# Kernel tuning notes

Hardware: AMD Instinct MI355X
Metric: run time of the kernel (lower is better)

Reference implementation:

```python
import jax, jax.numpy as jnp
import numpy as np

NUM_CLASSES = 10000
FEAT_DIM = 1024
BATCH = 4096


def setup_inputs() -> dict:
    key = jax.random.key(0)
    k1, k2 = jax.random.split(key)
    feat = jax.random.normal(k1, (BATCH, FEAT_DIM), dtype=jnp.float32)
    centers = jax.random.normal(k2, (NUM_CLASSES, FEAT_DIM), dtype=jnp.float32)
    return {"feat": feat, "centers": centers}


def reference(feat, centers):
    # logits = -0.5 * ||feat_b - center_c||^2, computed via the GEMM rewrite
    # ||a-b||^2 = ||a||^2 + ||b||^2 - 2 a.b  (same math as broadcast-sub-square-sum,
    # but avoids the [B, C, D] intermediate and uses tensor-core matmul).
    feat_sq = jnp.sum(feat * feat, axis=-1, keepdims=True)          # [B, 1]
    cent_sq = jnp.sum(centers * centers, axis=-1)[None, :]          # [1, C]
    cross = jnp.einsum('bd,cd->bc', feat, centers)                  # [B, C]
    dist = feat_sq + cent_sq - 2.0 * cross                          # [B, C]
    logits = -0.5 * dist
    return logits
```

## Files before the change

### kernel.cpp

```cpp
#include <hip/hip_runtime.h>
#include <hip/hip_bf16.h>
#include <stdint.h>

#define M_DIM 4096
#define N_DIM 10000
#define K_DIM 1024
#define GM (M_DIM / 128)
#define GN ((N_DIM + 127) / 128)
#define SB 16

typedef __attribute__((ext_vector_type(8))) short bf16x8;
typedef __attribute__((ext_vector_type(4))) float f32x4;

#define BAR()      asm volatile("s_barrier" ::: "memory")
#define WAITVM4()  asm volatile("s_waitcnt vmcnt(4)" ::: "memory")
#define WAITVM0()  asm volatile("s_waitcnt vmcnt(0)" ::: "memory")
#define WAITLGKM() asm volatile("s_waitcnt lgkmcnt(0)" ::: "memory")

__device__ __forceinline__ void async_ld16(const void* g, void* l) {
    __builtin_amdgcn_global_load_lds(
        (const __attribute__((address_space(1))) unsigned int*)g,
        (__attribute__((address_space(3))) unsigned int*)l,
        16, 0, 0);
}

__device__ __forceinline__ unsigned short f2bf(float f) {
    unsigned u = __float_as_uint(f);
    unsigned r = (u + 0x7FFFu + ((u >> 16) & 1u)) >> 16;
    return (unsigned short)r;
}

__global__ __launch_bounds__(256) void prep_rows(
    const float* __restrict__ feat, const float* __restrict__ cent,
    unsigned short* __restrict__ featbf, unsigned short* __restrict__ centbf,
    float* __restrict__ fsq, float* __restrict__ csq)
{
    const int wlane = threadIdx.x & 63;
    const int wid   = blockIdx.x * 4 + (threadIdx.x >> 6);
    const int nw    = gridDim.x * 4;
    for (int row = wid; row < M_DIM + N_DIM; row += nw) {
        const float* in;
        unsigned short* outb;
        float* sqp;
        if (row < M_DIM) {
            in = feat + (size_t)row * K_DIM;
            outb = featbf + (size_t)row * K_DIM;
            sqp = fsq + row;
        } else {
            const int r2 = row - M_DIM;
            in = cent + (size_t)r2 * K_DIM;
            outb = centbf + (size_t)r2 * K_DIM;
            sqp = csq + r2;
        }
        float s = 0.f;
        #pragma unroll
        for (int c = 0; c < 4; c++) {
            float4 v = ((const float4*)in)[wlane + c * 64];
            ushort4 pk;
            pk.x = f2bf(v.x); pk.y = f2bf(v.y); pk.z = f2bf(v.z); pk.w = f2bf(v.w);
            ((ushort4*)outb)[wlane + c * 64] = pk;
            s += v.x * v.x + v.y * v.y + v.z * v.z + v.w * v.w;
        }
        #pragma unroll
        for (int off = 32; off > 0; off >>= 1) s += __shfl_down(s, off, 64);
        if (wlane == 0) *sqp = s;
    }
}

__global__ __launch_bounds__(256) void gemm_bt(
    const unsigned short* __restrict__ A,
    const unsigned short* __restrict__ B,
    const float* __restrict__ fsq, const float* __restrict__ csq,
    float* __restrict__ out)
{
    __shared__ unsigned short smem[16384];

    const int tid  = threadIdx.x;
    const int lane = tid & 63;
    const int wave = tid >> 6;
    const int wm = wave & 1, wn = wave >> 1;

    const int lin  = blockIdx.x;
    const int band = lin / (SB * GM);
    const int r0   = lin - band * (SB * GM);
    const int bn0  = band * SB;
    int bw = GN - bn0; if (bw > SB) bw = SB;
    const int bm = r0 / bw;
    const int bn = bn0 + (r0 - bm * bw);

    const int arow_base = bm * 128;
    const int brow_base = bn * 128;

    const int srow = tid >> 2;
    const int scol = (tid & 3) * 8;

    const unsigned short* gA0 = A + (size_t)(arow_base + srow) * K_DIM + scol;
    const unsigned short* gA1 = gA0 + (size_t)64 * K_DIM;
    int br0 = brow_base + srow;      if (br0 > N_DIM - 1) br0 = N_DIM - 1;
    int br1 = brow_base + 64 + srow; if (br1 > N_DIM - 1) br1 = N_DIM - 1;
    const unsigned short* gB0 = B + (size_t)br0 * K_DIM + scol;
    const unsigned short* gB1 = B + (size_t)br1 * K_DIM + scol;

    f32x4 acc[4][4];
    #pragma unroll
    for (int i = 0; i < 4; i++)
        #pragma unroll
        for (int j = 0; j < 4; j++) {
            f32x4 z = {0.f, 0.f, 0.f, 0.f};
            acc[i][j] = z;
        }

    const int mlane = lane & 15;
    const int quad  = lane >> 4;
    const int aoff = (wm * 64 + mlane) * 32 + quad * 8;
    const int boff = 4096 + (wn * 64 + mlane) * 32 + quad * 8;

    async_ld16(gA0, smem + tid * 8);
    async_ld16(gA1, smem + 2048 + tid * 8);
    async_ld16(gB0, smem + 4096 + tid * 8);
    async_ld16(gB1, smem + 6144 + tid * 8);
    gA0 += 32; gA1 += 32; gB0 += 32; gB1 += 32;

    #define COMPUTE(bufbase)                                                  \
        do {                                                                  \
            const unsigned short* ap = smem + (bufbase) + aoff;               \
            const unsigned short* bp = smem + (bufbase) + boff;               \
            bf16x8 af[4], bfv[4];                                             \
            _Pragma("unroll")                                                 \
            for (int i = 0; i < 4; i++) {                                     \
                af[i]  = *(const bf16x8*)(ap + i * 16 * 32);                  \
                bfv[i] = *(const bf16x8*)(bp + i * 16 * 32);                  \
            }                                                                 \
            _Pragma("unroll")                                                 \
            for (int i = 0; i < 4; i++)                                       \
                _Pragma("unroll")                                             \
                for (int j = 0; j < 4; j++)                                   \
                    acc[i][j] = __builtin_amdgcn_mfma_f32_16x16x32_bf16(      \
                        af[i], bfv[j], acc[i][j], 0, 0, 0);                   \
        } while (0)

    for (int kt = 0; kt < K_DIM / 32 - 1; ++kt) {
        const int buf  = kt & 1;
        const int nbase = (buf ^ 1) * 8192;
        async_ld16(gA0, smem + nbase + tid * 8);
        async_ld16(gA1, smem + nbase + 2048 + tid * 8);
        async_ld16(gB0, smem + nbase + 4096 + tid * 8);
        async_ld16(gB1, smem + nbase + 6144 + tid * 8);
        gA0 += 32; gA1 += 32; gB0 += 32; gB1 += 32;
        WAITVM4();
        BAR();
        COMPUTE(buf * 8192);
        BAR();
    }
    WAITVM0();
    BAR();
    COMPUTE(8192);
    BAR();

    float* W = (float*)smem + wave * 1088;
    const int rbase0 = arow_base + wm * 64;
    const int cbase  = brow_base + wn * 64 + mlane;
    const int rb_col4 = mlane * 4;
    const int rb_rows = quad;
    const int gcol4 = brow_base + wn * 64 + rb_col4;
    const bool colok = gcol4 < N_DIM;

    #pragma unroll
    for (int i = 0; i < 4; i++) {
        float frow[4];
        #pragma unroll
        for (int r = 0; r < 4; r++)
            frow[r] = -0.5f * fsq[rbase0 + i * 16 + quad * 4 + r];
        #pragma unroll
        for (int j = 0; j < 4; j++) {
            int col = cbase + j * 16;
            float cs = -0.5f * csq[col < N_DIM ? col : (N_DIM - 1)];
            #pragma unroll
            for (int r = 0; r < 4; r++)
                W[(quad * 4 + r) * 68 + j * 16 + mlane] = acc[i][j][r] + frow[r] + cs;
        }
        WAITLGKM();
        #pragma unroll
        for (int s = 0; s < 4; s++) {
            int rl = s * 4 + rb_rows;
            f32x4 v = *(const f32x4*)&W[rl * 68 + rb_col4];
            if (colok) {
                int grow = rbase0 + i * 16 + rl;
                __builtin_nontemporal_store(v, (f32x4*)&out[(size_t)grow * N_DIM + gcol4]);
            }
        }
        WAITLGKM();
    }
    #undef COMPUTE
}

extern "C" void kernel_launch(void* const* d_in, const int* in_sizes, int n_in,
                              void* d_out, int out_size, void* d_ws, size_t ws_size,
                              hipStream_t stream) {
    const float* feat = (const float*)d_in[0];
    const float* cent = (const float*)d_in[1];
    float* out = (float*)d_out;

    char* ws = (char*)d_ws;
    unsigned short* featbf = (unsigned short*)ws;
    unsigned short* centbf = (unsigned short*)(ws + 8388608);
    float* fsq = (float*)(ws + 8388608 + 20480000);
    float* csq = (float*)(ws + 8388608 + 20480000 + 16384);

    prep_rows<<<1024, 256, 0, stream>>>(feat, cent, featbf, centbf, fsq, csq);

    gemm_bt<<<GM * GN, 256, 0, stream>>>(featbf, centbf, fsq, csq, out);
}
```

Before: 302.0 us.

## Enlarge GEMM tile to 256x256 with 8 waves, triple-buffered swizzled LDS

Switches the bf16 GEMM from 128x128 tiles with 4 waves to 256x256 tiles with 8 waves. It also adds a three-stage LDS ring with XOR-swizzled K offsets to avoid bank conflicts, and splits each K step into two half-compute phases that interleave the A and B prefetches. Blocks are remapped in XCD-aware order, and setprio is raised around the MFMA bursts. The aim is more operand reuse per loaded byte and better overlap of loads with compute. In exchange each block uses 96KB of LDS and more registers, which lowers occupancy. The 256-wide N tiling also wastes more work on the ragged 10000 edge.

After: 293.1 us. -2.9%, faster.

```diff
diff --git a/kernel.cpp b/kernel.cpp
--- a/kernel.cpp
+++ b/kernel.cpp
@@ -5,9 +5,9 @@
 #define M_DIM 4096
 #define N_DIM 10000
 #define K_DIM 1024
-#define GM (M_DIM / 128)
-#define GN ((N_DIM + 127) / 128)
-#define SB 16
+#define GM (M_DIM / 256)
+#define GN ((N_DIM + 255) / 256)
+#define NT (K_DIM / 32)
 
 typedef __attribute__((ext_vector_type(8))) short bf16x8;
 typedef __attribute__((ext_vector_type(4))) float f32x4;
@@ -67,106 +67,136 @@
     }
 }
 
-__global__ __launch_bounds__(256) void gemm_bt(
+__global__ __launch_bounds__(512, 2) void gemm_bt(
     const unsigned short* __restrict__ A,
     const unsigned short* __restrict__ B,
     const float* __restrict__ fsq, const float* __restrict__ csq,
     float* __restrict__ out)
 {
-    __shared__ unsigned short smem[16384];
+    __shared__ unsigned short smem[49152];
 
     const int tid  = threadIdx.x;
     const int lane = tid & 63;
     const int wave = tid >> 6;
-    const int wm = wave & 1, wn = wave >> 1;
-
-    const int lin  = blockIdx.x;
-    const int band = lin / (SB * GM);
-    const int r0   = lin - band * (SB * GM);
-    const int bn0  = band * SB;
-    int bw = GN - bn0; if (bw > SB) bw = SB;
-    const int bm = r0 / bw;
-    const int bn = bn0 + (r0 - bm * bw);
-
-    const int arow_base = bm * 128;
-    const int brow_base = bn * 128;
-
-    const int srow = tid >> 2;
-    const int scol = (tid & 3) * 8;
-
-    const unsigned short* gA0 = A + (size_t)(arow_base + srow) * K_DIM + scol;
-    const unsigned short* gA1 = gA0 + (size_t)64 * K_DIM;
-    int br0 = brow_base + srow;      if (br0 > N_DIM - 1) br0 = N_DIM - 1;
-    int br1 = brow_base + 64 + srow; if (br1 > N_DIM - 1) br1 = N_DIM - 1;
-    const unsigned short* gB0 = B + (size_t)br0 * K_DIM + scol;
-    const unsigned short* gB1 = B + (size_t)br1 * K_DIM + scol;
-
-    f32x4 acc[4][4];
+    const int wm = wave & 1;
+    const int wn = wave >> 1;
+    const int mlane = lane & 15;
+    const int quad  = lane >> 4;
+    const int fr  = (mlane >> 1) & 3;
+    const int qx  = (quad ^ fr) << 4;
+
+    const int bid = blockIdx.x;
+    const int xcd = bid & 7;
+    const int idx = bid >> 3;
+    const int r0  = xcd * 80 + idx;
+    const int bm  = r0 & 15;
+    const int bn  = r0 >> 4;
+
+    const int arow_base = bm * 256;
+    const int brow_base = bn * 256;
+
+    const unsigned short* gA[2];
+    const unsigned short* gB[2];
+    int ldsA[2], ldsB[2];
     #pragma unroll
-    for (int i = 0; i < 4; i++)
+    for (int i = 0; i < 2; i++) {
+        const int s   = i * 512 + tid;
+        const int row = s >> 2;
+        const int sc  = s & 3;
+        const int kof = (sc ^ ((row >> 1) & 3)) << 3;
+        gA[i] = A + (size_t)(arow_base + row) * K_DIM + kof;
+        int br = brow_base + row; if (br > N_DIM - 1) br = N_DIM - 1;
+        gB[i] = B + (size_t)br * K_DIM + kof;
+        ldsA[i] = s * 16;
+        ldsB[i] = 16384 + s * 16;
+    }
+
+    #define STAGE_A(t2, nbb)                                                  \
+        do {                                                                  \
+            async_ld16(gA[0] + (size_t)(t2) * 32, (char*)smem + (nbb) + ldsA[0]); \
+            async_ld16(gA[1] + (size_t)(t2) * 32, (char*)smem + (nbb) + ldsA[1]); \
+        } while (0)
+    #define STAGE_B(t2, nbb)                                                  \
+        do {                                                                  \
+            async_ld16(gB[0] + (size_t)(t2) * 32, (char*)smem + (nbb) + ldsB[0]); \
+            async_ld16(gB[1] + (size_t)(t2) * 32, (char*)smem + (nbb) + ldsB[1]); \
+        } while (0)
+
+    f32x4 acc[8][4];
+    #pragma unroll
+    for (int i = 0; i < 8; i++)
         #pragma unroll
         for (int j = 0; j < 4; j++) {
             f32x4 z = {0.f, 0.f, 0.f, 0.f};
             acc[i][j] = z;
         }
 
-    const int mlane = lane & 15;
-    const int quad  = lane >> 4;
-    const int aoff = (wm * 64 + mlane) * 32 + quad * 8;
-    const int boff = 4096 + (wn * 64 + mlane) * 32 + quad * 8;
-
-    async_ld16(gA0, smem + tid * 8);
-    async_ld16(gA1, smem + 2048 + tid * 8);
-    async_ld16(gB0, smem + 4096 + tid * 8);
-    async_ld16(gB1, smem + 6144 + tid * 8);
-    gA0 += 32; gA1 += 32; gB0 += 32; gB1 += 32;
-
-    #define COMPUTE(bufbase)                                                  \
-        do {                                                                  \
-            const unsigned short* ap = smem + (bufbase) + aoff;               \
-            const unsigned short* bp = smem + (bufbase) + boff;               \
-            bf16x8 af[4], bfv[4];                                             \
-            _Pragma("unroll")                                                 \
-            for (int i = 0; i < 4; i++) {                                     \
-                af[i]  = *(const bf16x8*)(ap + i * 16 * 32);                  \
-                bfv[i] = *(const bf16x8*)(bp + i * 16 * 32);                  \
-            }                                                                 \
-            _Pragma("unroll")                                                 \
-            for (int i = 0; i < 4; i++)                                       \
-                _Pragma("unroll")                                             \
-                for (int j = 0; j < 4; j++)                                   \
-                    acc[i][j] = __builtin_amdgcn_mfma_f32_16x16x32_bf16(      \
-                        af[i], bfv[j], acc[i][j], 0, 0, 0);                   \
-        } while (0)
-
-    for (int kt = 0; kt < K_DIM / 32 - 1; ++kt) {
-        const int buf  = kt & 1;
-        const int nbase = (buf ^ 1) * 8192;
-        async_ld16(gA0, smem + nbase + tid * 8);
-        async_ld16(gA1, smem + nbase + 2048 + tid * 8);
-        async_ld16(gB0, smem + nbase + 4096 + tid * 8);
-        async_ld16(gB1, smem + nbase + 6144 + tid * 8);
-        gA0 += 32; gA1 += 32; gB0 += 32; gB1 += 32;
-        WAITVM4();
-        BAR();
-        COMPUTE(buf * 8192);
-        BAR();
-    }
-    WAITVM0();
+    const int aBase = (wm * 128 + mlane) * 64 + qx;
+    const int bBase = 16384 + (wn * 64 + mlane) * 64 + qx;
+
+    STAGE_A(0, 0); STAGE_B(0, 0);
+    STAGE_A(1, 32768); STAGE_B(1, 32768);
+    WAITVM4();
     BAR();
-    COMPUTE(8192);
-    BAR();
+
+    int bb = 0;
+    for (int t = 0; t < NT; ++t) {
+        int nb = bb - 32768; if (nb < 0) nb = 65536;
+        const char* base = (const char*)smem + bb;
+        bf16x8 af[4], bfv[4];
+
+        #pragma unroll
+        for (int i = 0; i < 4; i++) {
+            af[i]  = *(const bf16x8*)(base + aBase + i * 1024);
+            bfv[i] = *(const bf16x8*)(base + bBase + i * 1024);
+        }
+        if (t + 2 < NT) STAGE_A(t + 2, nb);
+        BAR();
+        WAITLGKM();
+        __builtin_amdgcn_s_setprio(1);
+        #pragma unroll
+        for (int i = 0; i < 4; i++)
+            #pragma unroll
+            for (int j = 0; j < 4; j++)
+                acc[i][j] = __builtin_amdgcn_mfma_f32_16x16x32_bf16(
+                    af[i], bfv[j], acc[i][j], 0, 0, 0);
+        __builtin_amdgcn_s_setprio(0);
+        BAR();
+
+        #pragma unroll
+        for (int i = 0; i < 4; i++)
+            af[i] = *(const bf16x8*)(base + aBase + 4096 + i * 1024);
+        if (t + 2 < NT) STAGE_B(t + 2, nb);
+        BAR();
+        WAITLGKM();
+        __builtin_amdgcn_s_setprio(1);
+        #pragma unroll
+        for (int i = 0; i < 4; i++)
+            #pragma unroll
+            for (int j = 0; j < 4; j++)
+                acc[4 + i][j] = __builtin_amdgcn_mfma_f32_16x16x32_bf16(
+                    af[i], bfv[j], acc[4 + i][j], 0, 0, 0);
+        __builtin_amdgcn_s_setprio(0);
+
+        if (t < NT - 1) {
+            if (t + 2 < NT) { WAITVM4(); } else { WAITVM0(); }
+        }
+        BAR();
+
+        bb += 32768; if (bb > 65536) bb = 0;
+    }
+    #undef STAGE_A
+    #undef STAGE_B
 
     float* W = (float*)smem + wave * 1088;
-    const int rbase0 = arow_base + wm * 64;
+    const int rbase0 = arow_base + wm * 128;
     const int cbase  = brow_base + wn * 64 + mlane;
     const int rb_col4 = mlane * 4;
-    const int rb_rows = quad;
-    const int gcol4 = brow_base + wn * 64 + rb_col4;
+    const int gcol4  = brow_base + wn * 64 + rb_col4;
     const bool colok = gcol4 < N_DIM;
 
     #pragma unroll
-    for (int i = 0; i < 4; i++) {
+    for (int i = 0; i < 8; i++) {
         float frow[4];
         #pragma unroll
         for (int r = 0; r < 4; r++)
@@ -182,7 +212,7 @@
         WAITLGKM();
         #pragma unroll
         for (int s = 0; s < 4; s++) {
-            int rl = s * 4 + rb_rows;
+            int rl = s * 4 + quad;
             f32x4 v = *(const f32x4*)&W[rl * 68 + rb_col4];
             if (colok) {
                 int grow = rbase0 + i * 16 + rl;
@@ -191,7 +221,6 @@
         }
         WAITLGKM();
     }
-    #undef COMPUTE
 }
 
 extern "C" void kernel_launch(void* const* d_in, const int* in_sizes, int n_in,
@@ -209,5 +238,5 @@
 
     prep_rows<<<1024, 256, 0, stream>>>(feat, cent, featbf, centbf, fsq, csq);
 
-    gemm_bt<<<GM * GN, 256, 0, stream>>>(featbf, centbf, fsq, csq, out);
-}
+    gemm_bt<<<GM * GN, 512, 0, stream>>>(featbf, centbf, fsq, csq, out);
+}
```
